# Kernel tuning notes

Measured on AMD Instinct MI355X. Metric: run time of the kernel, lower is better.

Reference implementation:

```python
import jax, jax.numpy as jnp
import numpy as np

IN_SIZE = 512
UNITS = 512
GRID_SIZE = 5
ORDER = 3
LO, HI = -1.0, 1.0
BATCH = 1024


def _make_grid():
    # grid: (in_size, grid_size + 2*order + 1), extended beyond grid_range by order knot spacings
    bound = HI - LO
    g = jnp.linspace(LO - ORDER * bound / GRID_SIZE,
                     HI + ORDER * bound / GRID_SIZE,
                     GRID_SIZE + 2 * ORDER + 1, dtype=jnp.float32)
    return jnp.tile(g[None, :], (IN_SIZE, 1))


def _spline_bases(x, grid):
    # Cox-de Boor recursion. x: (B, in), grid: (in, G)
    xe = x[..., None]  # (B, in, 1)
    bases = ((xe >= grid[:, :-1]) & (xe < grid[:, 1:])).astype(x.dtype)  # order-0 indicators
    for k in range(1, ORDER + 1):
        left = (xe - grid[:, :-(k + 1)]) / (grid[:, k:-1] - grid[:, :-(k + 1)]) * bases[..., :-1]
        right = (grid[:, k + 1:] - xe) / (grid[:, k + 1:] - grid[:, 1:-k]) * bases[..., 1:]
        bases = left + right
    return bases  # (B, in, grid_size + order)


def setup_inputs() -> dict:
    key = jax.random.key(0)
    k1, k2, k3 = jax.random.split(key, 3)
    x = jax.random.normal(k1, (BATCH, IN_SIZE), jnp.float32)
    spline_kernel = 0.1 * jax.random.normal(k2, (IN_SIZE, GRID_SIZE + ORDER, UNITS), jnp.float32)
    limit = float(np.sqrt(6.0 / (IN_SIZE + UNITS)))  # GlorotUniform
    scale_factor = jax.random.uniform(k3, (IN_SIZE, UNITS), jnp.float32, -limit, limit)
    bias = jnp.zeros((UNITS,), jnp.float32)
    return {"x": x, "spline_kernel": spline_kernel, "scale_factor": scale_factor, "bias": bias}


def reference(x, spline_kernel, scale_factor, bias):
    grid = _make_grid()
    bases = _spline_bases(x, grid)                              # (B, in, basis)
    spline_out = jnp.einsum('bik,iko->bio', bases, spline_kernel)  # (B, in, units)
    spline_out = spline_out + jax.nn.silu(x)[..., None]            # add basis activation per feature
    spline_out = spline_out * scale_factor[None]                   # per (in, units) scaling
    out = jnp.sum(spline_out, axis=-2) + bias                      # reduce over in_size
    return out
```

## Files before the change

### kernel.cpp

```cpp
#include <hip/hip_runtime.h>
#include <cstdint>
#include <cmath>

typedef unsigned short u16;
typedef __bf16 bf16x8 __attribute__((ext_vector_type(8)));
typedef float f32x4 __attribute__((ext_vector_type(4)));

#define B_SZ   1024
#define IN_SZ  512
#define U_SZ   512
#define KTOT   4608
#define SPLITS 8
#define KLEN   576
#define KITERS 9

__device__ __forceinline__ u16 f2bf(float f) {
  __bf16 h = (__bf16)f;
  return __builtin_bit_cast(u16, h);
}

__device__ __forceinline__ void async16(const void* g, void* l) {
  __builtin_amdgcn_global_load_lds(
      (__attribute__((address_space(1))) void*)(g),
      (__attribute__((address_space(3))) void*)(l), 16u, 0, 0u);
}

__global__ void prep_w(const float* __restrict__ SK, const float* __restrict__ SF,
                       u16* __restrict__ WT) {
  __shared__ u16 tile[72 * 64];
  const int o0 = blockIdx.x * 64;
  const int i0 = blockIdx.y * 8;
  const int tid = threadIdx.x;
  const int oo = tid & 63, grp = tid >> 6;

  for (int tr = grp; tr < 72; tr += 4) {
    int i = i0 + tr / 9;
    int k = tr % 9;
    float sf = SF[(size_t)i * U_SZ + o0 + oo];
    float v  = (k < 8) ? SK[((size_t)i * 8 + k) * U_SZ + o0 + oo] * sf : sf;
    tile[tr * 64 + oo] = f2bf(v);
  }
  __syncthreads();

  const int t0 = i0 * 9;
  for (int idx = tid; idx < 72 * 64; idx += 256) {
    int ol = idx / 72;
    int c  = idx - ol * 72;
    WT[(size_t)(o0 + ol) * KTOT + t0 + c] = tile[c * 64 + ol];
  }
}

__global__ void bases_kernel(const float* __restrict__ X, u16* __restrict__ A) {
  const int gid = blockIdx.x * 256 + threadIdx.x;
  const float x = X[gid];

  const float T0 = -2.2f, H = 0.4f;
  float b0[11], b1[10], b2[9], b3[8];
#pragma unroll
  for (int j = 0; j < 11; ++j) {
    float tj  = T0 + H * j;
    float tj1 = T0 + H * (j + 1);
    b0[j] = (x >= tj && x < tj1) ? 1.0f : 0.0f;
  }
#pragma unroll
  for (int j = 0; j < 10; ++j) {
    float tj  = T0 + H * j;
    float tj2 = T0 + H * (j + 2);
    b1[j] = (x - tj) * 2.5f * b0[j] + (tj2 - x) * 2.5f * b0[j + 1];
  }
#pragma unroll
  for (int j = 0; j < 9; ++j) {
    float tj  = T0 + H * j;
    float tj3 = T0 + H * (j + 3);
    b2[j] = (x - tj) * 1.25f * b1[j] + (tj3 - x) * 1.25f * b1[j + 1];
  }
#pragma unroll
  for (int j = 0; j < 8; ++j) {
    float tj  = T0 + H * j;
    float tj4 = T0 + H * (j + 4);
    b3[j] = (x - tj) * (1.0f / 1.2f) * b2[j] + (tj4 - x) * (1.0f / 1.2f) * b2[j + 1];
  }
  float sil = x / (1.0f + expf(-x));

  u16* row = A + (size_t)gid * 9;
#pragma unroll
  for (int k = 0; k < 8; ++k) row[k] = f2bf(b3[k]);
  row[8] = f2bf(sil);
}

__global__ void __launch_bounds__(64) gemm_kan(const u16* __restrict__ A,
                                               const u16* __restrict__ WT,
                                               float* __restrict__ P) {
  __shared__ __align__(16) u16 sA[2][64 * 64];
  __shared__ __align__(16) u16 sB[2][64 * 64];

  const int lane  = threadIdx.x;
  const int m0    = blockIdx.x * 64;
  const int n0    = blockIdx.y * 64;
  const int sidx  = blockIdx.z;
  const int kbase = sidx * KLEN;

  const int r = lane >> 3, c = lane & 7;
  const u16* gA = A  + (size_t)(m0 + r) * KTOT + c * 8;
  const u16* gB = WT + (size_t)(n0 + r) * KTOT + c * 8;

  f32x4 acc[4][4];
#pragma unroll
  for (int i = 0; i < 4; ++i)
#pragma unroll
    for (int j = 0; j < 4; ++j) acc[i][j] = (f32x4)0.0f;

  {
    char* lA = (char*)(&sA[0][0]) + lane * 16;
    char* lB = (char*)(&sB[0][0]) + lane * 16;
#pragma unroll
    for (int j = 0; j < 8; ++j) {
      async16(gA + kbase + (size_t)j * 8 * KTOT, lA + j * 1024);
      async16(gB + kbase + (size_t)j * 8 * KTOT, lB + j * 1024);
    }
  }

  const int m = lane & 15, q = lane >> 4;
#pragma unroll
  for (int it = 0; it < KITERS; ++it) {
    const int cur = it & 1;
    __syncthreads();
    if (it + 1 < KITERS) {
      int k0 = kbase + (it + 1) * 64;
      char* lA = (char*)(&sA[cur ^ 1][0]) + lane * 16;
      char* lB = (char*)(&sB[cur ^ 1][0]) + lane * 16;
#pragma unroll
      for (int j = 0; j < 8; ++j) {
        async16(gA + k0 + (size_t)j * 8 * KTOT, lA + j * 1024);
        async16(gB + k0 + (size_t)j * 8 * KTOT, lB + j * 1024);
      }
    }
    const u16* At = &sA[cur][0];
    const u16* Bt = &sB[cur][0];
#pragma unroll
    for (int s = 0; s < 2; ++s) {
      bf16x8 af[4], bfv[4];
#pragma unroll
      for (int t = 0; t < 4; ++t)
        af[t] = *(const bf16x8*)(At + (t * 16 + m) * 64 + s * 32 + q * 8);
#pragma unroll
      for (int t = 0; t < 4; ++t)
        bfv[t] = *(const bf16x8*)(Bt + (t * 16 + m) * 64 + s * 32 + q * 8);
#pragma unroll
      for (int mt = 0; mt < 4; ++mt)
#pragma unroll
        for (int nt = 0; nt < 4; ++nt)
          acc[mt][nt] = __builtin_amdgcn_mfma_f32_16x16x32_bf16(
              af[mt], bfv[nt], acc[mt][nt], 0, 0, 0);
    }
  }

  float* Pp = P + (size_t)sidx * (B_SZ * U_SZ);
#pragma unroll
  for (int mt = 0; mt < 4; ++mt)
#pragma unroll
    for (int rr = 0; rr < 4; ++rr) {
      int row = m0 + mt * 16 + q * 4 + rr;
      size_t rb = (size_t)row * U_SZ + n0 + m;
#pragma unroll
      for (int nt = 0; nt < 4; ++nt) Pp[rb + nt * 16] = acc[mt][nt][rr];
    }
}

__global__ void reduce_kernel(const float* __restrict__ P,
                              const float* __restrict__ bias,
                              float* __restrict__ out) {
  const int idx = blockIdx.x * 256 + threadIdx.x;
  const f32x4* P4 = (const f32x4*)P;
  f32x4 acc = P4[idx];
#pragma unroll
  for (int s = 1; s < SPLITS; ++s) acc += P4[(size_t)s * (B_SZ * U_SZ / 4) + idx];
  acc += ((const f32x4*)bias)[idx & 127];
  ((f32x4*)out)[idx] = acc;
}

extern "C" void kernel_launch(void* const* d_in, const int* in_sizes, int n_in,
                              void* d_out, int out_size, void* d_ws, size_t ws_size,
                              hipStream_t stream) {
  const float* X    = (const float*)d_in[0];
  const float* SK   = (const float*)d_in[1];
  const float* SF   = (const float*)d_in[2];
  const float* bias = (const float*)d_in[3];

  char* ws = (char*)d_ws;
  u16*   WT = (u16*)ws;
  u16*   A  = (u16*)(ws + 4718592);
  float* P  = (float*)(ws + 4718592 + 9437184);

  hipLaunchKernelGGL(prep_w,        dim3(8, 64),   dim3(256), 0, stream, SK, SF, WT);
  hipLaunchKernelGGL(bases_kernel,  dim3(2048),    dim3(256), 0, stream, X, A);
  hipLaunchKernelGGL(gemm_kan,      dim3(16, 8, 8), dim3(64), 0, stream, A, WT, P);
  hipLaunchKernelGGL(reduce_kernel, dim3(512),     dim3(256), 0, stream, P, bias, (float*)d_out);
}
```

Baseline: 100.8 us.

## Use 4-wave 128x128 GEMM tiles with swizzled LDS and deeper split-K

Rewrites the split-K GEMM from one-wave 64x64 blocks into four-wave 128x128 blocks with a K step of 32. The shared-memory layout gets an XOR swizzle to cut bank conflicts on fragment reads. Split-K doubles from 8 to 16 so the grid still has enough blocks to fill the device. The cost is twice the partial-sum traffic written by the GEMM and read back by the reduce kernel, and a larger workspace for the partials.

After: 98.60 us. 1.02x faster.

```diff
diff --git a/kernel.cpp b/kernel.cpp
--- a/kernel.cpp
+++ b/kernel.cpp
@@ -10,8 +10,9 @@
 #define IN_SZ  512
 #define U_SZ   512
 #define KTOT   4608
-#define SPLITS 8
-#define KLEN   576
+#define SPLITS 16
+#define KLEN   288
+#define BK     32
 #define KITERS 9
 
 __device__ __forceinline__ u16 f2bf(float f) {
@@ -88,21 +89,29 @@
   row[8] = f2bf(sil);
 }
 
-__global__ void __launch_bounds__(64) gemm_kan(const u16* __restrict__ A,
-                                               const u16* __restrict__ WT,
-                                               float* __restrict__ P) {
-  __shared__ __align__(16) u16 sA[2][64 * 64];
-  __shared__ __align__(16) u16 sB[2][64 * 64];
-
-  const int lane  = threadIdx.x;
-  const int m0    = blockIdx.x * 64;
-  const int n0    = blockIdx.y * 64;
-  const int sidx  = blockIdx.z;
-  const int kbase = sidx * KLEN;
-
-  const int r = lane >> 3, c = lane & 7;
-  const u16* gA = A  + (size_t)(m0 + r) * KTOT + c * 8;
-  const u16* gB = WT + (size_t)(n0 + r) * KTOT + c * 8;
+__global__ void __launch_bounds__(256) gemm_kan(const u16* __restrict__ A,
+                                                const u16* __restrict__ WT,
+                                                float* __restrict__ P) {
+  __shared__ __align__(16) u16 sA[2][128 * BK];
+  __shared__ __align__(16) u16 sB[2][128 * BK];
+
+  const int t    = threadIdx.x;
+  const int lane = t & 63;
+  const int w    = t >> 6;
+  const int wr   = w >> 1;
+  const int wn   = w & 1;
+  const int m0   = blockIdx.x * 128;
+  const int n0   = blockIdx.y * 128;
+  const int kbase = blockIdx.z * KLEN;
+
+  const int srow = t >> 2, sc = t & 3;
+  const int sg0 = (sc ^ (srow & 3)) * 8;
+  const int srow1 = (t + 256) >> 2, sc1 = t & 3;
+  const int sg1 = (sc1 ^ (srow1 & 3)) * 8;
+  const u16* gA0 = A  + (size_t)(m0 + srow)  * KTOT + sg0;
+  const u16* gA1 = A  + (size_t)(m0 + srow1) * KTOT + sg1;
+  const u16* gB0 = WT + (size_t)(n0 + srow)  * KTOT + sg0;
+  const u16* gB1 = WT + (size_t)(n0 + srow1) * KTOT + sg1;
 
   f32x4 acc[4][4];
 #pragma unroll
@@ -110,58 +119,51 @@
 #pragma unroll
     for (int j = 0; j < 4; ++j) acc[i][j] = (f32x4)0.0f;
 
-  {
-    char* lA = (char*)(&sA[0][0]) + lane * 16;
-    char* lB = (char*)(&sB[0][0]) + lane * 16;
-#pragma unroll
-    for (int j = 0; j < 8; ++j) {
-      async16(gA + kbase + (size_t)j * 8 * KTOT, lA + j * 1024);
-      async16(gB + kbase + (size_t)j * 8 * KTOT, lB + j * 1024);
-    }
-  }
+  auto stage = [&](int buf, int k0) {
+    char* lA = (char*)(&sA[buf][0]) + t * 16;
+    char* lB = (char*)(&sB[buf][0]) + t * 16;
+    async16(gA0 + k0, lA);
+    async16(gA1 + k0, lA + 4096);
+    async16(gB0 + k0, lB);
+    async16(gB1 + k0, lB + 4096);
+  };
+
+  stage(0, kbase);
 
   const int m = lane & 15, q = lane >> 4;
+  const int qs = (q ^ (m & 3)) * 16;
+  const char* fA = (const char*)(&sA[0][0]) + (wr * 64 + m) * (BK * 2) + qs;
+  const char* fB = (const char*)(&sB[0][0]) + (wn * 64 + m) * (BK * 2) + qs;
+  const int bufstep = 128 * BK * 2;
+
 #pragma unroll
   for (int it = 0; it < KITERS; ++it) {
     const int cur = it & 1;
     __syncthreads();
-    if (it + 1 < KITERS) {
-      int k0 = kbase + (it + 1) * 64;
-      char* lA = (char*)(&sA[cur ^ 1][0]) + lane * 16;
-      char* lB = (char*)(&sB[cur ^ 1][0]) + lane * 16;
-#pragma unroll
-      for (int j = 0; j < 8; ++j) {
-        async16(gA + k0 + (size_t)j * 8 * KTOT, lA + j * 1024);
-        async16(gB + k0 + (size_t)j * 8 * KTOT, lB + j * 1024);
-      }
-    }
-    const u16* At = &sA[cur][0];
-    const u16* Bt = &sB[cur][0];
-#pragma unroll
-    for (int s = 0; s < 2; ++s) {
-      bf16x8 af[4], bfv[4];
-#pragma unroll
-      for (int t = 0; t < 4; ++t)
-        af[t] = *(const bf16x8*)(At + (t * 16 + m) * 64 + s * 32 + q * 8);
-#pragma unroll
-      for (int t = 0; t < 4; ++t)
-        bfv[t] = *(const bf16x8*)(Bt + (t * 16 + m) * 64 + s * 32 + q * 8);
-#pragma unroll
-      for (int mt = 0; mt < 4; ++mt)
-#pragma unroll
-        for (int nt = 0; nt < 4; ++nt)
-          acc[mt][nt] = __builtin_amdgcn_mfma_f32_16x16x32_bf16(
-              af[mt], bfv[nt], acc[mt][nt], 0, 0, 0);
-    }
-  }
-
-  float* Pp = P + (size_t)sidx * (B_SZ * U_SZ);
+    if (it + 1 < KITERS) stage(cur ^ 1, kbase + (it + 1) * BK);
+
+    bf16x8 af[4], bfv[4];
+#pragma unroll
+    for (int tt = 0; tt < 4; ++tt)
+      af[tt] = *(const bf16x8*)(fA + cur * bufstep + tt * 16 * (BK * 2));
+#pragma unroll
+    for (int tt = 0; tt < 4; ++tt)
+      bfv[tt] = *(const bf16x8*)(fB + cur * bufstep + tt * 16 * (BK * 2));
+#pragma unroll
+    for (int mt = 0; mt < 4; ++mt)
+#pragma unroll
+      for (int nt = 0; nt < 4; ++nt)
+        acc[mt][nt] = __builtin_amdgcn_mfma_f32_16x16x32_bf16(
+            af[mt], bfv[nt], acc[mt][nt], 0, 0, 0);
+  }
+
+  float* Pp = P + (size_t)blockIdx.z * (B_SZ * U_SZ);
 #pragma unroll
   for (int mt = 0; mt < 4; ++mt)
 #pragma unroll
     for (int rr = 0; rr < 4; ++rr) {
-      int row = m0 + mt * 16 + q * 4 + rr;
-      size_t rb = (size_t)row * U_SZ + n0 + m;
+      int row = m0 + wr * 64 + mt * 16 + q * 4 + rr;
+      size_t rb = (size_t)row * U_SZ + n0 + wn * 64 + m;
 #pragma unroll
       for (int nt = 0; nt < 4; ++nt) Pp[rb + nt * 16] = acc[mt][nt][rr];
     }
@@ -192,8 +194,8 @@
   u16*   A  = (u16*)(ws + 4718592);
   float* P  = (float*)(ws + 4718592 + 9437184);
 
-  hipLaunchKernelGGL(prep_w,        dim3(8, 64),   dim3(256), 0, stream, SK, SF, WT);
-  hipLaunchKernelGGL(bases_kernel,  dim3(2048),    dim3(256), 0, stream, X, A);
-  hipLaunchKernelGGL(gemm_kan,      dim3(16, 8, 8), dim3(64), 0, stream, A, WT, P);
-  hipLaunchKernelGGL(reduce_kernel, dim3(512),     dim3(256), 0, stream, P, bias, (float*)d_out);
-}
+  hipLaunchKernelGGL(prep_w,        dim3(8, 64),    dim3(256), 0, stream, SK, SF, WT);
+  hipLaunchKernelGGL(bases_kernel,  dim3(2048),     dim3(256), 0, stream, X, A);
+  hipLaunchKernelGGL(gemm_kan,      dim3(8, 4, 16), dim3(256), 0, stream, A, WT, P);
+  hipLaunchKernelGGL(reduce_kernel, dim3(512),      dim3(256), 0, stream, P, bias, (float*)d_out);
+}
```
